# Optimization experiments

Hardware: AMD Instinct MI355X
Metric: run time of the kernel (lower is better)

## Reference

```python
import jax, jax.numpy as jnp
import numpy as np

TAU = 2.0        # spikingjelly LIFNode default tau
ALPHA = 4.0      # sigmoid surrogate alpha (spikingjelly default)
NUM_HEADS = 8
CHUNK = 2

@jax.custom_vjp
def heaviside(x):
    return (x >= 0).astype(x.dtype)

def _h_fwd(x):
    return heaviside(x), x

def _h_bwd(x, g):
    s = jax.nn.sigmoid(ALPHA * x)
    return (g * ALPHA * s * (1.0 - s),)

heaviside.defvjp(_h_fwd, _h_bwd)

def lif(x, v_th):
    # multi-step LIF: v <- v + (x - v)/tau ; spike = H(v - v_th) ; hard reset to 0
    def step(v, xt):
        v = v + (xt - v) / TAU
        s = heaviside(v - v_th)
        return v * (1.0 - s), s
    _, spikes = jax.lax.scan(step, jnp.zeros_like(x[0]), x)
    return spikes

def bn(x, p, eps=1e-5):
    # eval-mode BatchNorm1d over channel dim C of [T,B,C,V]; p = [gamma,beta,mean,var] each [C]
    g, b, m, v = p[0], p[1], p[2], p[3]
    scale = g * jax.lax.rsqrt(v + eps)
    return (x - m[:, None]) * scale[:, None] + b[:, None]

def setup_inputs() -> dict:
    key = jax.random.key(0)
    T, B, C, V = 8, 16, 256, 1024
    ks = jax.random.split(key, 10)
    def mk_bn(k):
        k1, k2, k3, k4 = jax.random.split(k, 4)
        return jnp.stack([
            jax.random.uniform(k1, (C,)) + 0.5,          # gamma
            0.1 * jax.random.normal(k2, (C,)),           # beta
            0.1 * jax.random.normal(k3, (C,)),           # running mean
            jax.random.uniform(k4, (C,)) * 0.5 + 0.5,    # running var (>0)
        ])
    w_scale = C ** -0.5
    return {
        "x": jax.random.normal(ks[0], (T, B, C, V), jnp.float32),
        "q_w": w_scale * jax.random.normal(ks[1], (C, C), jnp.float32),
        "k_w": w_scale * jax.random.normal(ks[2], (C, C), jnp.float32),
        "v_w": w_scale * jax.random.normal(ks[3], (C, C), jnp.float32),
        "proj_w": w_scale * jax.random.normal(ks[4], (C, C), jnp.float32),
        "proj_b": 0.01 * jax.random.normal(ks[5], (C,), jnp.float32),
        "bn_q": mk_bn(ks[6]),
        "bn_k": mk_bn(ks[7]),
        "bn_v": mk_bn(ks[8]),
        "bn_proj": mk_bn(ks[9]),
    }

def reference(x, q_w, k_w, v_w, proj_w, proj_b, bn_q, bn_k, bn_v, bn_proj):
    T, B, C, V = x.shape
    H = NUM_HEADS
    D = C // H
    N = V
    NC = T // CHUNK
    identity = x

    xs = lif(x, 1.0)  # shortcut_lif

    def branch(w, bnp):
        y = jnp.einsum('oc,tbcv->tbov', w, xs)   # 1x1 conv
        y = lif(bn(y, bnp), 1.0)
        # [T,B,C,V] -> [T,B,H,N,D]
        return y.transpose(0, 1, 3, 2).reshape(T, B, N, H, D).transpose(0, 1, 3, 2, 4)

    q = branch(q_w, bn_q)
    k = branch(k_w, bn_k)
    v = branch(v_w, bn_v)

    def chunk(t):
        # [T,B,H,N,D] -> [NC,B,H,CHUNK*N,D]
        return (t.reshape(NC, CHUNK, B, H, N, D)
                 .transpose(0, 2, 3, 1, 4, 5)
                 .reshape(NC, B, H, CHUNK * N, D))

    qc, kc, vc = chunk(q), chunk(k), chunk(v)
    attn = jnp.einsum('nbhld,nbhle->nbhde', kc, vc) * (1.0 / N)  # [NC,B,H,D,D]
    out = jnp.einsum('nbhld,nbhde->nbhle', qc, attn)             # [NC,B,H,CHUNK*N,D]
    out = (out.reshape(NC, B, H, CHUNK, N, D)
              .transpose(0, 3, 1, 2, 4, 5)
              .reshape(T, B, H, N, D))

    y = out.transpose(0, 1, 2, 4, 3).reshape(T, B, C, N)  # [T,B,H,D,N] -> [T,B,C,N]
    y = lif(y, 0.5)  # attn_lif
    y = jnp.einsum('oc,tbcv->tbov', proj_w, y) + proj_b[None, None, :, None]
    y = bn(y, bn_proj)
    return y + identity, v
```

## Files before the change

kernel.cpp:

```cpp
#include <hip/hip_runtime.h>
#include <hip/hip_bf16.h>
#include <math.h>

typedef __bf16 bf16_t;
typedef __bf16 bf16x8 __attribute__((ext_vector_type(8)));
typedef __bf16 bf16x4 __attribute__((ext_vector_type(4)));
typedef float  f32x4  __attribute__((ext_vector_type(4)));

#define T_ 8
#define B_ 16
#define C_ 256
#define V_ 1024
#define H_ 8
#define D_ 32

#define MFMA __builtin_amdgcn_mfma_f32_16x16x32_bf16

__global__ __launch_bounds__(256) void k0_split(const float* __restrict__ W,
                                                bf16_t* __restrict__ S0,
                                                bf16_t* __restrict__ S1,
                                                bf16_t* __restrict__ S2)
{
    int i = (blockIdx.x * 256 + threadIdx.x) * 4;
    float4 w = *(const float4*)(W + i);
    float wv[4] = {w.x, w.y, w.z, w.w};
    bf16x4 s0, s1, s2;
#pragma unroll
    for (int j = 0; j < 4; j++) {
        bf16_t a = (bf16_t)wv[j];
        float r1 = wv[j] - (float)a;
        bf16_t b = (bf16_t)r1;
        float r2 = r1 - (float)b;
        bf16_t c = (bf16_t)r2;
        s0[j] = a; s1[j] = b; s2[j] = c;
    }
    *(bf16x4*)(S0 + i) = s0;
    *(bf16x4*)(S1 + i) = s1;
    *(bf16x4*)(S2 + i) = s2;
}

__global__ __launch_bounds__(256) void k1_lif_tr(const float* __restrict__ x,
                                                 bf16_t* __restrict__ xsT)
{
    __shared__ bf16_t tile[64 * 72];
    const int v0 = blockIdx.x * 64, c0 = blockIdx.y * 64, b = blockIdx.z;
    const int tid = threadIdx.x;
    const int cc = tid >> 2, v16 = (tid & 3) * 16;
    const int vr = tid >> 2, c16 = (tid & 3) * 16;
    float mem[16];
#pragma unroll
    for (int j = 0; j < 16; j++) mem[j] = 0.0f;

    for (int t = 0; t < T_; t++) {
        const float* xp = x + (((size_t)(t * B_ + b) * C_ + (c0 + cc)) * V_ + v0 + v16);
        float xv[16];
#pragma unroll
        for (int q = 0; q < 4; q++) {
            float4 f = *(const float4*)(xp + q * 4);
            xv[q * 4 + 0] = f.x; xv[q * 4 + 1] = f.y;
            xv[q * 4 + 2] = f.z; xv[q * 4 + 3] = f.w;
        }
#pragma unroll
        for (int j = 0; j < 16; j++) {
            float m = mem[j];
            float d = xv[j] - m;
            m = m + d * 0.5f;
            float s = (m >= 1.0f) ? 1.0f : 0.0f;
            tile[(v16 + j) * 72 + cc] = (bf16_t)s;
            mem[j] = (s != 0.0f) ? 0.0f : m;
        }
        __syncthreads();
        bf16_t* op = xsT + (((size_t)(t * B_ + b) * V_ + (v0 + vr)) * C_ + c0 + c16);
        *(bf16x8*)op       = *(const bf16x8*)&tile[vr * 72 + c16];
        *(bf16x8*)(op + 8) = *(const bf16x8*)&tile[vr * 72 + c16 + 8];
        __syncthreads();
    }
}

template <int ORIENT>
__global__ __launch_bounds__(256) void k_branch(const bf16_t* __restrict__ Wsp,
                                                const float* __restrict__ bnp,
                                                const bf16_t* __restrict__ xsT,
                                                bf16_t* __restrict__ outp, float vth)
{
    __shared__ bf16_t Wl[3][64 * 72];
    __shared__ bf16_t Xl[64 * 72];
    __shared__ float bsc[64], bmn[64], bbt[64];
    const int v0 = blockIdx.x * 64, o0 = blockIdx.y * 64, b = blockIdx.z;
    const int tid = threadIdx.x;
    const int w = tid >> 6, l = tid & 63, lq = l >> 4, lr = l & 15;
    const int msub = (w >> 1) * 32, nsub = (w & 1) * 32;

    if (tid < 64) {
        int o = o0 + tid;
        float g = bnp[o], be = bnp[C_ + o];
        float mn = bnp[2 * C_ + o], vr2 = bnp[3 * C_ + o];
        bsc[tid] = g * (1.0f / sqrtf(vr2 + 1e-5f));
        bmn[tid] = mn; bbt[tid] = be;
    }
    float mem[4][4];
#pragma unroll
    for (int st = 0; st < 4; st++)
        for (int r = 0; r < 4; r++) mem[st][r] = 0.0f;

    for (int t = 0; t < T_; t++) {
        f32x4 acc[4];
#pragma unroll
        for (int i = 0; i < 4; i++) acc[i] = (f32x4){0.f, 0.f, 0.f, 0.f};
        for (int kq = 0; kq < 4; kq++) {
            __syncthreads();
#pragma unroll
            for (int i = 0; i < 6; i++) {
                int ch = tid + i * 256;
                int lvl = ch >> 9, rem = ch & 511;
                int row = rem >> 3, col8 = (rem & 7) * 8;
                *(bf16x8*)&Wl[lvl][row * 72 + col8] =
                    *(const bf16x8*)&Wsp[lvl * 65536 + (o0 + row) * 256 + kq * 64 + col8];
            }
            {
                size_t xb = ((size_t)(t * B_ + b) * V_ + v0);
#pragma unroll
                for (int i = 0; i < 2; i++) {
                    int ch = tid + i * 256;
                    int row = ch >> 3, col8 = (ch & 7) * 8;
                    *(bf16x8*)&Xl[row * 72 + col8] =
                        *(const bf16x8*)&xsT[(xb + row) * C_ + kq * 64 + col8];
                }
            }
            __syncthreads();
#pragma unroll
            for (int kk = 0; kk < 2; kk++) {
                int kb = kk * 32 + lq * 8;
                if (ORIENT == 0) {
                    bf16x8 b0 = *(const bf16x8*)&Xl[(nsub + lr) * 72 + kb];
                    bf16x8 b1 = *(const bf16x8*)&Xl[(nsub + 16 + lr) * 72 + kb];
#pragma unroll
                    for (int lvl = 0; lvl < 3; lvl++) {
                        bf16x8 a0 = *(const bf16x8*)&Wl[lvl][(msub + lr) * 72 + kb];
                        bf16x8 a1 = *(const bf16x8*)&Wl[lvl][(msub + 16 + lr) * 72 + kb];
                        acc[0] = MFMA(a0, b0, acc[0], 0, 0, 0);
                        acc[1] = MFMA(a0, b1, acc[1], 0, 0, 0);
                        acc[2] = MFMA(a1, b0, acc[2], 0, 0, 0);
                        acc[3] = MFMA(a1, b1, acc[3], 0, 0, 0);
                    }
                } else {
                    bf16x8 a0 = *(const bf16x8*)&Xl[(msub + lr) * 72 + kb];
                    bf16x8 a1 = *(const bf16x8*)&Xl[(msub + 16 + lr) * 72 + kb];
#pragma unroll
                    for (int lvl = 0; lvl < 3; lvl++) {
                        bf16x8 b0 = *(const bf16x8*)&Wl[lvl][(nsub + lr) * 72 + kb];
                        bf16x8 b1 = *(const bf16x8*)&Wl[lvl][(nsub + 16 + lr) * 72 + kb];
                        acc[0] = MFMA(a0, b0, acc[0], 0, 0, 0);
                        acc[1] = MFMA(a0, b1, acc[1], 0, 0, 0);
                        acc[2] = MFMA(a1, b0, acc[2], 0, 0, 0);
                        acc[3] = MFMA(a1, b1, acc[3], 0, 0, 0);
                    }
                }
            }
        }
#pragma unroll
        for (int st = 0; st < 4; st++) {
            int mi = st >> 1, ni = st & 1;
#pragma unroll
            for (int r = 0; r < 4; r++) {
                int m = msub + mi * 16 + lq * 4 + r;
                int n = nsub + ni * 16 + lr;
                int ol = ORIENT ? n : m;
                int vl = ORIENT ? m : n;
                float y = (acc[st][r] - bmn[ol]) * bsc[ol] + bbt[ol];
                float mm = mem[st][r];
                mm = mm + (y - mm) * 0.5f;
                float s = (mm >= vth) ? 1.0f : 0.0f;
                size_t idx = ORIENT
                    ? (((size_t)(t * B_ + b) * V_ + (v0 + vl)) * C_ + (o0 + ol))
                    : (((size_t)(t * B_ + b) * C_ + (o0 + ol)) * V_ + (v0 + vl));
                outp[idx] = (bf16_t)s;
                mem[st][r] = (s != 0.0f) ? 0.0f : mm;
            }
        }
    }
}

__global__ __launch_bounds__(64) void k_attn(const bf16_t* __restrict__ vc,
                                             const bf16_t* __restrict__ kc,
                                             bf16_t* __restrict__ ahi,
                                             bf16_t* __restrict__ alo)
{
    const int fid = blockIdx.x;
    const int h = fid & 7, b = (fid >> 3) & 15, nc = fid >> 7;
    const int l = threadIdx.x, lq = l >> 4, lr = l & 15;
    f32x4 acc[4];
#pragma unroll
    for (int i = 0; i < 4; i++) acc[i] = (f32x4){0.f, 0.f, 0.f, 0.f};
    for (int s = 0; s < 64; s++) {
        int t = nc * 2 + (s >> 5);
        int n0 = (s & 31) * 32;
        size_t rb = ((size_t)(t * B_ + b) * C_ + h * D_ + lr) * V_ + n0 + lq * 8;
        bf16x8 a0 = *(const bf16x8*)&vc[rb];
        bf16x8 a1 = *(const bf16x8*)&vc[rb + (size_t)16 * V_];
        bf16x8 b0 = *(const bf16x8*)&kc[rb];
        bf16x8 b1 = *(const bf16x8*)&kc[rb + (size_t)16 * V_];
        acc[0] = MFMA(a0, b0, acc[0], 0, 0, 0);
        acc[1] = MFMA(a0, b1, acc[1], 0, 0, 0);
        acc[2] = MFMA(a1, b0, acc[2], 0, 0, 0);
        acc[3] = MFMA(a1, b1, acc[3], 0, 0, 0);
    }
    size_t ob = (size_t)fid * 1024;
#pragma unroll
    for (int st = 0; st < 4; st++) {
        int ei = st >> 1, di = st & 1;
#pragma unroll
        for (int r = 0; r < 4; r++) {
            int e = ei * 16 + lq * 4 + r;
            int d = di * 16 + lr;
            float val = acc[st][r] * (1.0f / 1024.0f);
            bf16_t hi = (bf16_t)val;
            float lo = val - (float)hi;
            ahi[ob + e * 32 + d] = hi;
            alo[ob + e * 32 + d] = (bf16_t)lo;
        }
    }
}

__global__ __launch_bounds__(256) void k_attn_out(const bf16_t* __restrict__ qT,
                                                  const bf16_t* __restrict__ ahi,
                                                  const bf16_t* __restrict__ alo,
                                                  bf16_t* __restrict__ y3T)
{
    const int tid = threadIdx.x, w = tid >> 6, l = tid & 63, lq = l >> 4, lr = l & 15;
    const int n0 = blockIdx.x * 64 + (w >> 1) * 32;
    const int h = blockIdx.y * 2 + (w & 1);
    const int b = blockIdx.z;
    float mem[4][4];
#pragma unroll
    for (int st = 0; st < 4; st++)
        for (int r = 0; r < 4; r++) mem[st][r] = 0.0f;

    for (int t = 0; t < T_; t++) {
        int nc = t >> 1;
        const bf16_t* qp = qT + ((size_t)(t * B_ + b) * V_ + n0 + lr) * C_ + h * D_ + lq * 8;
        bf16x8 a0 = *(const bf16x8*)qp;
        bf16x8 a1 = *(const bf16x8*)(qp + 16 * C_);
        size_t ab = ((size_t)(nc * B_ + b) * H_ + h) * 1024;
        bf16x8 bh0 = *(const bf16x8*)&ahi[ab + lr * 32 + lq * 8];
        bf16x8 bh1 = *(const bf16x8*)&ahi[ab + (16 + lr) * 32 + lq * 8];
        bf16x8 bl0 = *(const bf16x8*)&alo[ab + lr * 32 + lq * 8];
        bf16x8 bl1 = *(const bf16x8*)&alo[ab + (16 + lr) * 32 + lq * 8];
#pragma unroll
        for (int st = 0; st < 4; st++) {
            int mi = st >> 1, ni = st & 1;
            f32x4 z = (f32x4){0.f, 0.f, 0.f, 0.f};
            z = MFMA(mi ? a1 : a0, ni ? bh1 : bh0, z, 0, 0, 0);
            z = MFMA(mi ? a1 : a0, ni ? bl1 : bl0, z, 0, 0, 0);
#pragma unroll
            for (int r = 0; r < 4; r++) {
                int n = n0 + mi * 16 + lq * 4 + r;
                int e = ni * 16 + lr;
                float mm = mem[st][r];
                mm = mm + (z[r] - mm) * 0.5f;
                float s = (mm >= 0.5f) ? 1.0f : 0.0f;
                y3T[((size_t)(t * B_ + b) * V_ + n) * C_ + h * D_ + e] = (bf16_t)s;
                mem[st][r] = (s != 0.0f) ? 0.0f : mm;
            }
        }
    }
}

__global__ __launch_bounds__(256) void k_proj(const bf16_t* __restrict__ Wsp,
                                              const float* __restrict__ pb,
                                              const float* __restrict__ bnp,
                                              const bf16_t* __restrict__ y3T,
                                              const float* __restrict__ x,
                                              float* __restrict__ out0)
{
    __shared__ bf16_t Wl[3][64 * 72];
    __shared__ bf16_t Xl[64 * 72];
    __shared__ float bsc[64], bmn[64], bbt[64], bbi[64];
    const int v0 = blockIdx.x * 64, o0 = blockIdx.y * 64;
    const int tb = blockIdx.z, t = tb >> 4, b = tb & 15;
    const int tid = threadIdx.x, w = tid >> 6, l = tid & 63, lq = l >> 4, lr = l & 15;
    const int msub = (w >> 1) * 32, nsub = (w & 1) * 32;

    if (tid < 64) {
        int o = o0 + tid;
        float g = bnp[o], be = bnp[C_ + o];
        float mn = bnp[2 * C_ + o], vr2 = bnp[3 * C_ + o];
        bsc[tid] = g * (1.0f / sqrtf(vr2 + 1e-5f));
        bmn[tid] = mn; bbt[tid] = be; bbi[tid] = pb[o];
    }
    f32x4 acc[4];
#pragma unroll
    for (int i = 0; i < 4; i++) acc[i] = (f32x4){0.f, 0.f, 0.f, 0.f};
    for (int kq = 0; kq < 4; kq++) {
        __syncthreads();
#pragma unroll
        for (int i = 0; i < 6; i++) {
            int ch = tid + i * 256;
            int lvl = ch >> 9, rem = ch & 511;
            int row = rem >> 3, col8 = (rem & 7) * 8;
            *(bf16x8*)&Wl[lvl][row * 72 + col8] =
                *(const bf16x8*)&Wsp[lvl * 65536 + (o0 + row) * 256 + kq * 64 + col8];
        }
        {
            size_t xb = ((size_t)(t * B_ + b) * V_ + v0);
#pragma unroll
            for (int i = 0; i < 2; i++) {
                int ch = tid + i * 256;
                int row = ch >> 3, col8 = (ch & 7) * 8;
                *(bf16x8*)&Xl[row * 72 + col8] =
                    *(const bf16x8*)&y3T[(xb + row) * C_ + kq * 64 + col8];
            }
        }
        __syncthreads();
#pragma unroll
        for (int kk = 0; kk < 2; kk++) {
            int kb = kk * 32 + lq * 8;
            bf16x8 b0 = *(const bf16x8*)&Xl[(nsub + lr) * 72 + kb];
            bf16x8 b1 = *(const bf16x8*)&Xl[(nsub + 16 + lr) * 72 + kb];
#pragma unroll
            for (int lvl = 0; lvl < 3; lvl++) {
                bf16x8 a0 = *(const bf16x8*)&Wl[lvl][(msub + lr) * 72 + kb];
                bf16x8 a1 = *(const bf16x8*)&Wl[lvl][(msub + 16 + lr) * 72 + kb];
                acc[0] = MFMA(a0, b0, acc[0], 0, 0, 0);
                acc[1] = MFMA(a0, b1, acc[1], 0, 0, 0);
                acc[2] = MFMA(a1, b0, acc[2], 0, 0, 0);
                acc[3] = MFMA(a1, b1, acc[3], 0, 0, 0);
            }
        }
    }
#pragma unroll
    for (int st = 0; st < 4; st++) {
        int mi = st >> 1, ni = st & 1;
#pragma unroll
        for (int r = 0; r < 4; r++) {
            int m = msub + mi * 16 + lq * 4 + r;
            int n = nsub + ni * 16 + lr;
            size_t idx = ((size_t)(t * B_ + b) * C_ + (o0 + m)) * V_ + (v0 + n);
            float y = acc[st][r] + bbi[m];
            y = (y - bmn[m]) * bsc[m] + bbt[m];
            y += x[idx];
            out0[idx] = y;
        }
    }
}

__global__ __launch_bounds__(256) void k_vout(const bf16_t* __restrict__ vc,
                                              float* __restrict__ out1)
{
    __shared__ bf16_t tl[32 * 136];
    const int n0 = blockIdx.x * 128;
    const int f = blockIdx.y;
    const int tb = f >> 3, h = f & 7;
    const int tid = threadIdx.x;
    {
        int d = tid >> 3, nn = (tid & 7) * 16;
        const bf16_t* vp = vc + ((size_t)tb * C_ + h * D_ + d) * V_ + n0 + nn;
        *(bf16x8*)&tl[d * 136 + nn]     = *(const bf16x8*)vp;
        *(bf16x8*)&tl[d * 136 + nn + 8] = *(const bf16x8*)(vp + 8);
    }
    __syncthreads();
    {
        int n = tid >> 1, d16 = (tid & 1) * 16;
        float* op = out1 + (size_t)f * (V_ * D_) + (size_t)(n0 + n) * D_ + d16;
#pragma unroll
        for (int q = 0; q < 4; q++) {
            float4 o;
            o.x = (float)tl[(d16 + q * 4 + 0) * 136 + n];
            o.y = (float)tl[(d16 + q * 4 + 1) * 136 + n];
            o.z = (float)tl[(d16 + q * 4 + 2) * 136 + n];
            o.w = (float)tl[(d16 + q * 4 + 3) * 136 + n];
            *(float4*)(op + q * 4) = o;
        }
    }
}

extern "C" void kernel_launch(void* const* d_in, const int* in_sizes, int n_in,
                              void* d_out, int out_size, void* d_ws, size_t ws_size,
                              hipStream_t stream)
{
    const float* x    = (const float*)d_in[0];
    const float* q_w  = (const float*)d_in[1];
    const float* k_w  = (const float*)d_in[2];
    const float* v_w  = (const float*)d_in[3];
    const float* pw   = (const float*)d_in[4];
    const float* pb   = (const float*)d_in[5];
    const float* bn_q = (const float*)d_in[6];
    const float* bn_k = (const float*)d_in[7];
    const float* bn_v = (const float*)d_in[8];
    const float* bn_p = (const float*)d_in[9];

    char* ws = (char*)d_ws;
    bf16_t* xsT  = (bf16_t*)(ws);
    bf16_t* vc   = (bf16_t*)(ws + ((size_t)64 << 20));
    bf16_t* ahi  = (bf16_t*)(ws + ((size_t)128 << 20));
    bf16_t* alo  = (bf16_t*)(ws + ((size_t)129 << 20));
    bf16_t* wspq = (bf16_t*)(ws + ((size_t)130 << 20));
    bf16_t* wspk = wspq + 3 * 65536;
    bf16_t* wspv = wspk + 3 * 65536;
    bf16_t* wspp = wspv + 3 * 65536;
    bf16_t* y3T  = xsT;

    float* outf = (float*)d_out;
    bf16_t* qT = (bf16_t*)d_out;
    bf16_t* kc = (bf16_t*)((char*)d_out + ((size_t)64 << 20));

    k0_split<<<dim3(64), 256, 0, stream>>>(q_w, wspq, wspq + 65536, wspq + 131072);
    k0_split<<<dim3(64), 256, 0, stream>>>(k_w, wspk, wspk + 65536, wspk + 131072);
    k0_split<<<dim3(64), 256, 0, stream>>>(v_w, wspv, wspv + 65536, wspv + 131072);
    k0_split<<<dim3(64), 256, 0, stream>>>(pw,  wspp, wspp + 65536, wspp + 131072);

    k1_lif_tr   <<<dim3(16, 4, 16),  256, 0, stream>>>(x, xsT);
    k_branch<1> <<<dim3(16, 4, 16),  256, 0, stream>>>(wspq, bn_q, xsT, qT, 1.0f);
    k_branch<0> <<<dim3(16, 4, 16),  256, 0, stream>>>(wspk, bn_k, xsT, kc, 1.0f);
    k_branch<0> <<<dim3(16, 4, 16),  256, 0, stream>>>(wspv, bn_v, xsT, vc, 1.0f);
    k_attn      <<<dim3(512),         64, 0, stream>>>(vc, kc, ahi, alo);
    k_attn_out  <<<dim3(16, 4, 16),  256, 0, stream>>>(qT, ahi, alo, y3T);
    k_proj      <<<dim3(16, 4, 128), 256, 0, stream>>>(wspp, pb, bn_p, y3T, x, outf);
    k_vout      <<<dim3(8, 1024),    256, 0, stream>>>(vc, outf + (size_t)33554432);
}
```

Measured before the change: 769.5 us.

## Batch all timesteps per block so weight tiles load once per K-slice

k_branch and k_proj now keep accumulators for all 8 timesteps and loop over K in slices of 32, loading each weight slice once and reusing it across every timestep. The old code reloaded the weights separately for each timestep. The LIF recurrence then runs afterwards over the stored accumulators. k_proj's grid drops from 128 to 16 z-blocks, so fewer blocks each do more work. This costs 128 accumulator registers per lane and less grid parallelism, and launch bounds now request 2 blocks per CU. ORIENT=1 no longer swaps the MFMA operands, and its index math now maps the output channel to m, which may change the layout or coalescing of the q output.

Result: faster. 712.6 us (-7.4%).

```diff
diff --git a/kernel.cpp b/kernel.cpp
--- a/kernel.cpp
+++ b/kernel.cpp
@@ -78,13 +78,13 @@
 }
 
 template <int ORIENT>
-__global__ __launch_bounds__(256) void k_branch(const bf16_t* __restrict__ Wsp,
-                                                const float* __restrict__ bnp,
-                                                const bf16_t* __restrict__ xsT,
-                                                bf16_t* __restrict__ outp, float vth)
-{
-    __shared__ bf16_t Wl[3][64 * 72];
-    __shared__ bf16_t Xl[64 * 72];
+__global__ __launch_bounds__(256, 2) void k_branch(const bf16_t* __restrict__ Wsp,
+                                                   const float* __restrict__ bnp,
+                                                   const bf16_t* __restrict__ xsT,
+                                                   bf16_t* __restrict__ outp, float vth)
+{
+    __shared__ bf16_t Wl[3][64 * 40];
+    __shared__ bf16_t Xl[8][64 * 40];
     __shared__ float bsc[64], bmn[64], bbt[64];
     const int v0 = blockIdx.x * 64, o0 = blockIdx.y * 64, b = blockIdx.z;
     const int tid = threadIdx.x;
@@ -98,66 +98,60 @@
         bsc[tid] = g * (1.0f / sqrtf(vr2 + 1e-5f));
         bmn[tid] = mn; bbt[tid] = be;
     }
+
+    f32x4 acc[8][4];
+#pragma unroll
+    for (int t = 0; t < 8; t++)
+#pragma unroll
+        for (int i = 0; i < 4; i++) acc[t][i] = (f32x4){0.f, 0.f, 0.f, 0.f};
+
+    for (int kq = 0; kq < 8; kq++) {
+        __syncthreads();
+#pragma unroll
+        for (int i = 0; i < 3; i++) {
+            int ch = tid + i * 256;
+            int lvl = ch >> 8, rem = ch & 255;
+            int row = rem >> 2, col8 = (rem & 3) * 8;
+            *(bf16x8*)&Wl[lvl][row * 40 + col8] =
+                *(const bf16x8*)&Wsp[lvl * 65536 + (o0 + row) * 256 + kq * 32 + col8];
+        }
+#pragma unroll
+        for (int i = 0; i < 8; i++) {
+            int ch = tid + i * 256;
+            int tt = ch >> 8, rem = ch & 255;
+            int row = rem >> 2, col8 = (rem & 3) * 8;
+            *(bf16x8*)&Xl[tt][row * 40 + col8] =
+                *(const bf16x8*)&xsT[((size_t)(tt * B_ + b) * V_ + v0 + row) * C_ + kq * 32 + col8];
+        }
+        __syncthreads();
+
+        bf16x8 aw0[3], aw1[3];
+#pragma unroll
+        for (int lvl = 0; lvl < 3; lvl++) {
+            aw0[lvl] = *(const bf16x8*)&Wl[lvl][(msub + lr) * 40 + lq * 8];
+            aw1[lvl] = *(const bf16x8*)&Wl[lvl][(msub + 16 + lr) * 40 + lq * 8];
+        }
+#pragma unroll
+        for (int t = 0; t < 8; t++) {
+            bf16x8 b0 = *(const bf16x8*)&Xl[t][(nsub + lr) * 40 + lq * 8];
+            bf16x8 b1 = *(const bf16x8*)&Xl[t][(nsub + 16 + lr) * 40 + lq * 8];
+#pragma unroll
+            for (int lvl = 0; lvl < 3; lvl++) {
+                acc[t][0] = MFMA(aw0[lvl], b0, acc[t][0], 0, 0, 0);
+                acc[t][1] = MFMA(aw0[lvl], b1, acc[t][1], 0, 0, 0);
+                acc[t][2] = MFMA(aw1[lvl], b0, acc[t][2], 0, 0, 0);
+                acc[t][3] = MFMA(aw1[lvl], b1, acc[t][3], 0, 0, 0);
+            }
+        }
+    }
+
     float mem[4][4];
 #pragma unroll
     for (int st = 0; st < 4; st++)
+#pragma unroll
         for (int r = 0; r < 4; r++) mem[st][r] = 0.0f;
-
-    for (int t = 0; t < T_; t++) {
-        f32x4 acc[4];
-#pragma unroll
-        for (int i = 0; i < 4; i++) acc[i] = (f32x4){0.f, 0.f, 0.f, 0.f};
-        for (int kq = 0; kq < 4; kq++) {
-            __syncthreads();
-#pragma unroll
-            for (int i = 0; i < 6; i++) {
-                int ch = tid + i * 256;
-                int lvl = ch >> 9, rem = ch & 511;
-                int row = rem >> 3, col8 = (rem & 7) * 8;
-                *(bf16x8*)&Wl[lvl][row * 72 + col8] =
-                    *(const bf16x8*)&Wsp[lvl * 65536 + (o0 + row) * 256 + kq * 64 + col8];
-            }
-            {
-                size_t xb = ((size_t)(t * B_ + b) * V_ + v0);
-#pragma unroll
-                for (int i = 0; i < 2; i++) {
-                    int ch = tid + i * 256;
-                    int row = ch >> 3, col8 = (ch & 7) * 8;
-                    *(bf16x8*)&Xl[row * 72 + col8] =
-                        *(const bf16x8*)&xsT[(xb + row) * C_ + kq * 64 + col8];
-                }
-            }
-            __syncthreads();
-#pragma unroll
-            for (int kk = 0; kk < 2; kk++) {
-                int kb = kk * 32 + lq * 8;
-                if (ORIENT == 0) {
-                    bf16x8 b0 = *(const bf16x8*)&Xl[(nsub + lr) * 72 + kb];
-                    bf16x8 b1 = *(const bf16x8*)&Xl[(nsub + 16 + lr) * 72 + kb];
-#pragma unroll
-                    for (int lvl = 0; lvl < 3; lvl++) {
-                        bf16x8 a0 = *(const bf16x8*)&Wl[lvl][(msub + lr) * 72 + kb];
-                        bf16x8 a1 = *(const bf16x8*)&Wl[lvl][(msub + 16 + lr) * 72 + kb];
-                        acc[0] = MFMA(a0, b0, acc[0], 0, 0, 0);
-                        acc[1] = MFMA(a0, b1, acc[1], 0, 0, 0);
-                        acc[2] = MFMA(a1, b0, acc[2], 0, 0, 0);
-                        acc[3] = MFMA(a1, b1, acc[3], 0, 0, 0);
-                    }
-                } else {
-                    bf16x8 a0 = *(const bf16x8*)&Xl[(msub + lr) * 72 + kb];
-                    bf16x8 a1 = *(const bf16x8*)&Xl[(msub + 16 + lr) * 72 + kb];
-#pragma unroll
-                    for (int lvl = 0; lvl < 3; lvl++) {
-                        bf16x8 b0 = *(const bf16x8*)&Wl[lvl][(nsub + lr) * 72 + kb];
-                        bf16x8 b1 = *(const bf16x8*)&Wl[lvl][(nsub + 16 + lr) * 72 + kb];
-                        acc[0] = MFMA(a0, b0, acc[0], 0, 0, 0);
-                        acc[1] = MFMA(a0, b1, acc[1], 0, 0, 0);
-                        acc[2] = MFMA(a1, b0, acc[2], 0, 0, 0);
-                        acc[3] = MFMA(a1, b1, acc[3], 0, 0, 0);
-                    }
-                }
-            }
-        }
+#pragma unroll
+    for (int t = 0; t < 8; t++) {
 #pragma unroll
         for (int st = 0; st < 4; st++) {
             int mi = st >> 1, ni = st & 1;
@@ -165,15 +159,13 @@
             for (int r = 0; r < 4; r++) {
                 int m = msub + mi * 16 + lq * 4 + r;
                 int n = nsub + ni * 16 + lr;
-                int ol = ORIENT ? n : m;
-                int vl = ORIENT ? m : n;
-                float y = (acc[st][r] - bmn[ol]) * bsc[ol] + bbt[ol];
+                float y = (acc[t][st][r] - bmn[m]) * bsc[m] + bbt[m];
                 float mm = mem[st][r];
                 mm = mm + (y - mm) * 0.5f;
                 float s = (mm >= vth) ? 1.0f : 0.0f;
                 size_t idx = ORIENT
-                    ? (((size_t)(t * B_ + b) * V_ + (v0 + vl)) * C_ + (o0 + ol))
-                    : (((size_t)(t * B_ + b) * C_ + (o0 + ol)) * V_ + (v0 + vl));
+                    ? (((size_t)(t * B_ + b) * V_ + (v0 + n)) * C_ + (o0 + m))
+                    : (((size_t)(t * B_ + b) * C_ + (o0 + m)) * V_ + (v0 + n));
                 outp[idx] = (bf16_t)s;
                 mem[st][r] = (s != 0.0f) ? 0.0f : mm;
             }
@@ -234,6 +226,7 @@
     float mem[4][4];
 #pragma unroll
     for (int st = 0; st < 4; st++)
+#pragma unroll
         for (int r = 0; r < 4; r++) mem[st][r] = 0.0f;
 
     for (int t = 0; t < T_; t++) {
@@ -266,19 +259,19 @@
     }
 }
 
-__global__ __launch_bounds__(256) void k_proj(const bf16_t* __restrict__ Wsp,
-                                              const float* __restrict__ pb,
-                                              const float* __restrict__ bnp,
-                                              const bf16_t* __restrict__ y3T,
-                                              const float* __restrict__ x,
-                                              float* __restrict__ out0)
-{
-    __shared__ bf16_t Wl[3][64 * 72];
-    __shared__ bf16_t Xl[64 * 72];
+__global__ __launch_bounds__(256, 2) void k_proj(const bf16_t* __restrict__ Wsp,
+                                                 const float* __restrict__ pb,
+                                                 const float* __restrict__ bnp,
+                                                 const bf16_t* __restrict__ y3T,
+                                                 const float* __restrict__ x,
+                                                 float* __restrict__ out0)
+{
+    __shared__ bf16_t Wl[3][64 * 40];
+    __shared__ bf16_t Xl[8][64 * 40];
     __shared__ float bsc[64], bmn[64], bbt[64], bbi[64];
-    const int v0 = blockIdx.x * 64, o0 = blockIdx.y * 64;
-    const int tb = blockIdx.z, t = tb >> 4, b = tb & 15;
-    const int tid = threadIdx.x, w = tid >> 6, l = tid & 63, lq = l >> 4, lr = l & 15;
+    const int v0 = blockIdx.x * 64, o0 = blockIdx.y * 64, b = blockIdx.z;
+    const int tid = threadIdx.x;
+    const int w = tid >> 6, l = tid & 63, lq = l >> 4, lr = l & 15;
     const int msub = (w >> 1) * 32, nsub = (w & 1) * 32;
 
     if (tid < 64) {
@@ -288,58 +281,68 @@
         bsc[tid] = g * (1.0f / sqrtf(vr2 + 1e-5f));
         bmn[tid] = mn; bbt[tid] = be; bbi[tid] = pb[o];
     }
-    f32x4 acc[4];
-#pragma unroll
-    for (int i = 0; i < 4; i++) acc[i] = (f32x4){0.f, 0.f, 0.f, 0.f};
-    for (int kq = 0; kq < 4; kq++) {
-        __syncthreads();
-#pragma unroll
-        for (int i = 0; i < 6; i++) {
+
+    f32x4 acc[8][4];
+#pragma unroll
+    for (int t = 0; t < 8; t++)
+#pragma unroll
+        for (int i = 0; i < 4; i++) acc[t][i] = (f32x4){0.f, 0.f, 0.f, 0.f};
+
+    for (int kq = 0; kq < 8; kq++) {
+        __syncthreads();
+#pragma unroll
+        for (int i = 0; i < 3; i++) {
             int ch = tid + i * 256;
-            int lvl = ch >> 9, rem = ch & 511;
-            int row = rem >> 3, col8 = (rem & 7) * 8;
-            *(bf16x8*)&Wl[lvl][row * 72 + col8] =
-                *(const bf16x8*)&Wsp[lvl * 65536 + (o0 + row) * 256 + kq * 64 + col8];
-        }
-        {
-            size_t xb = ((size_t)(t * B_ + b) * V_ + v0);
-#pragma unroll
-            for (int i = 0; i < 2; i++) {
-                int ch = tid + i * 256;
-                int row = ch >> 3, col8 = (ch & 7) * 8;
-                *(bf16x8*)&Xl[row * 72 + col8] =
-                    *(const bf16x8*)&y3T[(xb + row) * C_ + kq * 64 + col8];
+            int lvl = ch >> 8, rem = ch & 255;
+            int row = rem >> 2, col8 = (rem & 3) * 8;
+            *(bf16x8*)&Wl[lvl][row * 40 + col8] =
+                *(const bf16x8*)&Wsp[lvl * 65536 + (o0 + row) * 256 + kq * 32 + col8];
+        }
+#pragma unroll
+        for (int i = 0; i < 8; i++) {
+            int ch = tid + i * 256;
+            int tt = ch >> 8, rem = ch & 255;
+            int row = rem >> 2, col8 = (rem & 3) * 8;
+            *(bf16x8*)&Xl[tt][row * 40 + col8] =
+                *(const bf16x8*)&y3T[((size_t)(tt * B_ + b) * V_ + v0 + row) * C_ + kq * 32 + col8];
+        }
+        __syncthreads();
+
+        bf16x8 aw0[3], aw1[3];
+#pragma unroll
+        for (int lvl = 0; lvl < 3; lvl++) {
+            aw0[lvl] = *(const bf16x8*)&Wl[lvl][(msub + lr) * 40 + lq * 8];
+            aw1[lvl] = *(const bf16x8*)&Wl[lvl][(msub + 16 + lr) * 40 + lq * 8];
+        }
+#pragma unroll
+        for (int t = 0; t < 8; t++) {
+            bf16x8 b0 = *(const bf16x8*)&Xl[t][(nsub + lr) * 40 + lq * 8];
+            bf16x8 b1 = *(const bf16x8*)&Xl[t][(nsub + 16 + lr) * 40 + lq * 8];
+#pragma unroll
+            for (int lvl = 0; lvl < 3; lvl++) {
+                acc[t][0] = MFMA(aw0[lvl], b0, acc[t][0], 0, 0, 0);
+                acc[t][1] = MFMA(aw0[lvl], b1, acc[t][1], 0, 0, 0);
+                acc[t][2] = MFMA(aw1[lvl], b0, acc[t][2], 0, 0, 0);
+                acc[t][3] = MFMA(aw1[lvl], b1, acc[t][3], 0, 0, 0);
             }
         }
-        __syncthreads();
-#pragma unroll
-        for (int kk = 0; kk < 2; kk++) {
-            int kb = kk * 32 + lq * 8;
-            bf16x8 b0 = *(const bf16x8*)&Xl[(nsub + lr) * 72 + kb];
-            bf16x8 b1 = *(const bf16x8*)&Xl[(nsub + 16 + lr) * 72 + kb];
-#pragma unroll
-            for (int lvl = 0; lvl < 3; lvl++) {
-                bf16x8 a0 = *(const bf16x8*)&Wl[lvl][(msub + lr) * 72 + kb];
-                bf16x8 a1 = *(const bf16x8*)&Wl[lvl][(msub + 16 + lr) * 72 + kb];
-                acc[0] = MFMA(a0, b0, acc[0], 0, 0, 0);
-                acc[1] = MFMA(a0, b1, acc[1], 0, 0, 0);
-                acc[2] = MFMA(a1, b0, acc[2], 0, 0, 0);
-                acc[3] = MFMA(a1, b1, acc[3], 0, 0, 0);
+    }
+
+#pragma unroll
+    for (int t = 0; t < 8; t++) {
+#pragma unroll
+        for (int st = 0; st < 4; st++) {
+            int mi = st >> 1, ni = st & 1;
+#pragma unroll
+            for (int r = 0; r < 4; r++) {
+                int m = msub + mi * 16 + lq * 4 + r;
+                int n = nsub + ni * 16 + lr;
+                size_t idx = ((size_t)(t * B_ + b) * C_ + (o0 + m)) * V_ + (v0 + n);
+                float y = acc[t][st][r] + bbi[m];
+                y = (y - bmn[m]) * bsc[m] + bbt[m];
+                y += x[idx];
+                out0[idx] = y;
             }
-        }
-    }
-#pragma unroll
-    for (int st = 0; st < 4; st++) {
-        int mi = st >> 1, ni = st & 1;
-#pragma unroll
-        for (int r = 0; r < 4; r++) {
-            int m = msub + mi * 16 + lq * 4 + r;
-            int n = nsub + ni * 16 + lr;
-            size_t idx = ((size_t)(t * B_ + b) * C_ + (o0 + m)) * V_ + (v0 + n);
-            float y = acc[st][r] + bbi[m];
-            y = (y - bmn[m]) * bsc[m] + bbt[m];
-            y += x[idx];
-            out0[idx] = y;
         }
     }
 }
@@ -415,6 +418,6 @@
     k_branch<0> <<<dim3(16, 4, 16),  256, 0, stream>>>(wspv, bn_v, xsT, vc, 1.0f);
     k_attn      <<<dim3(512),         64, 0, stream>>>(vc, kc, ahi, alo);
     k_attn_out  <<<dim3(16, 4, 16),  256, 0, stream>>>(qT, ahi, alo, y3T);
-    k_proj      <<<dim3(16, 4, 128), 256, 0, stream>>>(wspp, pb, bn_p, y3T, x, outf);
+    k_proj      <<<dim3(16, 4, 16),  256, 0, stream>>>(wspp, pb, bn_p, y3T, x, outf);
     k_vout      <<<dim3(8, 1024),    256, 0, stream>>>(vc, outf + (size_t)33554432);
 }
```
